# Performance work log

Measured on AMD Instinct MI355X. Metric: run time of the kernel, lower is better.

## Reference

```python
import jax, jax.numpy as jnp
import numpy as np

B, D, H, E, TOPK, NTASK = 16384, 128, 4, 8, 2, 1
ODIM = D // H  # MoE expert output dim (input_feat // num_heads)


def setup_inputs() -> dict:
    key = jax.random.key(0)
    ks = jax.random.split(key, 12)
    s = lambda k, shp, fan: jax.random.normal(k, shp, jnp.float32) / np.sqrt(fan)
    return {
        "x": jax.random.normal(ks[0], (B, D), jnp.float32),
        "Wq": s(ks[1], (D, D * H), D), "bq": jnp.zeros((D * H,), jnp.float32),
        "Wk": s(ks[2], (D, D * H), D), "bk": jnp.zeros((D * H,), jnp.float32),
        "Wg": s(ks[3], (D, E), D),
        "W1": s(ks[4], (E, D, D), D), "b1": jnp.zeros((E, D), jnp.float32),
        "W2": s(ks[5], (E, D, ODIM), D), "b2": jnp.zeros((E, ODIM), jnp.float32),
        "Wout": s(ks[6], (H * ODIM, NTASK), H * ODIM),
        "bout": jnp.zeros((NTASK,), jnp.float32),
    }


def reference(x, Wq, bq, Wk, bk, Wg, W1, b1, W2, b2, Wout, bout):
    # query/key projections -> [B, H, D] token views, flattened to [N, D]
    tok = (x @ Wq + bq).reshape(B * H, D)
    gate_tok = (x @ Wk + bk).reshape(B * H, D)

    # gating: softmax over experts, top-2 routing with renormalized weights
    probs = jax.nn.softmax(gate_tok @ Wg, axis=-1)          # [N, E]
    top_p, top_i = jax.lax.top_k(probs, TOPK)               # [N, k]
    weights = top_p / jnp.sum(top_p, axis=-1, keepdims=True)

    # expert MLPs (dense all-expert compute, then gather selected)
    h = jax.nn.relu(jnp.einsum('nd,edh->neh', tok, W1) + b1)  # [N, E, D]
    eo = jnp.einsum('neh,eho->neo', h, W2) + b2               # [N, E, ODIM]
    sel = jnp.take_along_axis(eo, top_i[:, :, None], axis=1)  # [N, k, ODIM]
    y = jnp.sum(weights[:, :, None] * sel, axis=1)            # [N, ODIM]

    # load-balancing auxiliary loss (switch-style): E * sum(frac_i * mean_prob_i)
    one_hot = jax.nn.one_hot(top_i[:, 0], E, dtype=probs.dtype)
    frac = jnp.mean(one_hot, axis=0)
    mean_p = jnp.mean(probs, axis=0)
    aux_loss = E * jnp.sum(frac * mean_p)

    out = y.reshape(B, H * ODIM) @ Wout + bout                # [B, NTASK]
    return out, aux_loss
```

## Files before the change

kernel.cpp:

```cpp
#include <hip/hip_runtime.h>
#include <hip/hip_bf16.h>

#define BB   16384
#define DD   128
#define HH   4
#define EE   8
#define NN   (BB*HH)
#define OD   32
#define PT   136
#define NL   32
#define CAP2 6144

typedef __attribute__((ext_vector_type(8))) short short8;
typedef __attribute__((ext_vector_type(4))) short short4v;
typedef __attribute__((ext_vector_type(4))) float f32x4;

static __device__ __forceinline__ short f2bf(float v) {
    unsigned int u = __builtin_bit_cast(unsigned int, v);
    u = (u + 0x7FFFu + ((u >> 16) & 1u)) >> 16;
    return (short)u;
}
static __device__ __forceinline__ float bf2f(short b) {
    unsigned int u = ((unsigned int)(unsigned short)b) << 16;
    return __builtin_bit_cast(float, u);
}

__global__ __launch_bounds__(256) void prep_tiny(
    const float* __restrict__ Wk, const float* __restrict__ Wg,
    const float* __restrict__ bk, const float* __restrict__ bout,
    float* __restrict__ Wkg, float* __restrict__ bkg,
    float* __restrict__ out, int* __restrict__ cursors)
{
    int idx = blockIdx.x * 256 + threadIdx.x;
    if (idx < 4096) {
        int k = idx >> 5, col = idx & 31, hh = col >> 3, e = col & 7;
        float s = 0.f;
        #pragma unroll 8
        for (int d = 0; d < 128; ++d) s += Wk[k * 512 + hh * 128 + d] * Wg[d * 8 + e];
        Wkg[k * 32 + col] = s;
    } else if (idx < 4128) {
        int r = idx - 4096;
        int hh = r >> 3, e = r & 7;
        float s = 0.f;
        #pragma unroll 8
        for (int d = 0; d < 128; ++d) s += bk[hh * 128 + d] * Wg[d * 8 + e];
        bkg[r] = s;
    } else if (idx < 20512) {
        out[idx - 4128] = bout[0];
    } else if (idx < 20544) {
        int r = idx - 20512;
        cursors[r] = r * CAP2;
    }
}

__global__ __launch_bounds__(256) void mid(
    const float* __restrict__ x, const float* __restrict__ Wq, const float* __restrict__ bq,
    const float* __restrict__ W1, const float* __restrict__ b1, const float* __restrict__ W2,
    const float* __restrict__ Wkg, const float* __restrict__ bkg,
    short* __restrict__ xb, short* __restrict__ A1F, float* __restrict__ bias1,
    short* __restrict__ W2F, float* __restrict__ wts, float* __restrict__ blkPart,
    int* __restrict__ cursors, int* __restrict__ listIdx)
{
    __shared__ __align__(16) char smemU[34816];
    __shared__ float lps[EE];
    __shared__ float lcn[EE];
    __shared__ int   lcnt[NL];
    __shared__ int   lbase[NL];

    const int blk = blockIdx.x;
    const int t   = threadIdx.x;

    if (blk < 256) {
        float* xL = (float*)smemU;
        const int b0 = blk * 64;

        if (t < EE) { lps[t] = 0.f; lcn[t] = 0.f; }
        if (t < NL) lcnt[t] = 0;

        for (int i = t; i < 2048; i += 256) {
            int r = i >> 5, c = i & 31;
            float4 v = ((const float4*)(x + (size_t)(b0 + r) * 128))[c];
            float* dst = xL + r * 129 + c * 4;
            dst[0] = v.x; dst[1] = v.y; dst[2] = v.z; dst[3] = v.w;
        }
        __syncthreads();

        const int h  = __builtin_amdgcn_readfirstlane(t >> 6);
        const int lb = t & 63;

        const f32x4* wkg4 = (const f32x4*)Wkg;
        f32x4 a0 = ((const f32x4*)bkg)[h * 2];
        f32x4 a1 = ((const f32x4*)bkg)[h * 2 + 1];

        const float* xrow = xL + lb * 129;
        #pragma unroll 4
        for (int k = 0; k < 128; ++k) {
            float xv = xrow[k];
            f32x4 w0 = wkg4[k * 8 + h * 2];
            f32x4 w1 = wkg4[k * 8 + h * 2 + 1];
            a0 += w0 * xv;
            a1 += w1 * xv;
        }

        float l[8] = {a0[0], a0[1], a0[2], a0[3], a1[0], a1[1], a1[2], a1[3]};
        float mx = l[0];
        #pragma unroll
        for (int e = 1; e < 8; ++e) mx = fmaxf(mx, l[e]);
        float p[8]; float sm = 0.f;
        #pragma unroll
        for (int e = 0; e < 8; ++e) { p[e] = __expf(l[e] - mx); sm += p[e]; }
        float isin = 1.f / sm;
        #pragma unroll
        for (int e = 0; e < 8; ++e) p[e] *= isin;

        int i1 = 0; float p1 = p[0];
        #pragma unroll
        for (int e = 1; e < 8; ++e) if (p[e] > p1) { p1 = p[e]; i1 = e; }
        int i2 = (i1 == 0) ? 1 : 0; float p2 = p[i2];
        #pragma unroll
        for (int e = 0; e < 8; ++e) if (e != i1 && p[e] > p2) { p2 = p[e]; i2 = e; }

        int n = (b0 + lb) * 4 + h;
        float rinv = 1.f / (p1 + p2);
        wts[2*n]    = p1 * rinv; wts[2*n+1]  = p2 * rinv;

        int li0 = i1 * 4 + h, li1 = i2 * 4 + h;
        int s0 = atomicAdd(&lcnt[li0], 1);
        int s1 = atomicAdd(&lcnt[li1], 1);

        #pragma unroll
        for (int e = 0; e < 8; ++e) {
            float v = p[e];
            #pragma unroll
            for (int m2 = 1; m2 < 64; m2 <<= 1) v += __shfl_xor(v, m2);
            unsigned long long m1b = __ballot(i1 == e);
            if (lb == 0) {
                atomicAdd(&lps[e], v);
                atomicAdd(&lcn[e], (float)__popcll(m1b));
            }
        }
        __syncthreads();
        if (t < NL) lbase[t] = atomicAdd(&cursors[t], lcnt[t]);
        __syncthreads();

        int q0 = lbase[li0] + s0;
        if (q0 < (li0 + 1) * CAP2) listIdx[q0] = 2*n;
        int q1 = lbase[li1] + s1;
        if (q1 < (li1 + 1) * CAP2) listIdx[q1] = 2*n + 1;

        if (t < EE) {
            float* bp = blkPart + blk * 16;
            bp[t]     = lps[t];
            bp[8 + t] = lcn[t];
        }
    } else if (blk < 288) {
        short* L = (short*)smemU;
        const int li = blk - 256;
        const int e = li >> 2, h = li & 3;
        const int wv = t >> 6, lane = t & 63, l16 = lane & 15, quad = lane >> 4;

        #pragma unroll
        for (int rep = 0; rep < 16; ++rep) {
            int idx = t + rep * 256;
            int c = idx >> 5, h4 = (idx & 31) * 4;
            float4 v = *(const float4*)(W1 + e * 16384 + c * 128 + h4);
            L[(h4 + 0) * PT + c] = f2bf(v.x);
            L[(h4 + 1) * PT + c] = f2bf(v.y);
            L[(h4 + 2) * PT + c] = f2bf(v.z);
            L[(h4 + 3) * PT + c] = f2bf(v.w);
        }
        __syncthreads();

        short8 af[2][4];
        #pragma unroll
        for (int ml = 0; ml < 2; ++ml)
            #pragma unroll
            for (int ks = 0; ks < 4; ++ks)
                af[ml][ks] = *(const short8*)(L + ((wv*2 + ml)*16 + l16) * PT + ks*32 + quad*8);
        if (t < 128) {
            float s = 0.f;
            #pragma unroll 8
            for (int c = 0; c < 128; ++c)
                s += bq[h*128 + c] * bf2f(L[t * PT + c]);
            bias1[li*128 + t] = s + b1[e*128 + t];
        }
        __syncthreads();

        #pragma unroll
        for (int rep = 0; rep < 4; ++rep) {
            int idx = t + rep * 256;
            int d = idx >> 3, c0 = (idx & 7) * 16;
            const float4* src = (const float4*)(Wq + d * 512 + h * 128 + c0);
            float4 v0 = src[0], v1 = src[1], v2 = src[2], v3 = src[3];
            short8 a, b;
            a[0]=f2bf(v0.x); a[1]=f2bf(v0.y); a[2]=f2bf(v0.z); a[3]=f2bf(v0.w);
            a[4]=f2bf(v1.x); a[5]=f2bf(v1.y); a[6]=f2bf(v1.z); a[7]=f2bf(v1.w);
            b[0]=f2bf(v2.x); b[1]=f2bf(v2.y); b[2]=f2bf(v2.z); b[3]=f2bf(v2.w);
            b[4]=f2bf(v3.x); b[5]=f2bf(v3.y); b[6]=f2bf(v3.z); b[7]=f2bf(v3.w);
            *(short8*)(L + d * PT + c0)     = a;
            *(short8*)(L + d * PT + c0 + 8) = b;
        }
        __syncthreads();

        f32x4 acc[2][8];
        #pragma unroll
        for (int ml = 0; ml < 2; ++ml)
            #pragma unroll
            for (int nt2 = 0; nt2 < 8; ++nt2)
                acc[ml][nt2] = (f32x4){0.f, 0.f, 0.f, 0.f};
        #pragma unroll
        for (int ks = 0; ks < 4; ++ks) {
            short8 bfr[8];
            #pragma unroll
            for (int nt2 = 0; nt2 < 8; ++nt2)
                bfr[nt2] = *(const short8*)(L + (nt2*16 + l16) * PT + ks*32 + quad*8);
            #pragma unroll
            for (int ml = 0; ml < 2; ++ml)
                #pragma unroll
                for (int nt2 = 0; nt2 < 8; ++nt2)
                    acc[ml][nt2] = __builtin_amdgcn_mfma_f32_16x16x32_bf16(af[ml][ks], bfr[nt2], acc[ml][nt2], 0, 0, 0);
        }
        __syncthreads();

        #pragma unroll
        for (int ml = 0; ml < 2; ++ml)
            #pragma unroll
            for (int nt2 = 0; nt2 < 8; ++nt2)
                #pragma unroll
                for (int r = 0; r < 4; ++r)
                    L[((wv*2 + ml)*16 + quad*4 + r) * PT + nt2*16 + l16] = f2bf(acc[ml][nt2][r]);
        __syncthreads();

        #pragma unroll
        for (int mt = 0; mt < 8; ++mt)
            #pragma unroll
            for (int ks = 0; ks < 4; ++ks) {
                short8 v = *(const short8*)(L + (mt*16 + l16) * PT + ks*32 + quad*8);
                *(short8*)(A1F + ((size_t)(((li*8 + mt)*4 + ks)*64 + lane)) * 8) = v;
            }
    } else {
        for (int s = blk - 288; s < 1152; s += 896) {
            if (s < 1024) {
                int idx = s * 256 + t;
                const float4* x4 = (const float4*)x;
                float4 v0 = x4[idx * 2], v1 = x4[idx * 2 + 1];
                short8 sv;
                sv[0]=f2bf(v0.x); sv[1]=f2bf(v0.y); sv[2]=f2bf(v0.z); sv[3]=f2bf(v0.w);
                sv[4]=f2bf(v1.x); sv[5]=f2bf(v1.y); sv[6]=f2bf(v1.z); sv[7]=f2bf(v1.w);
                *(short8*)(xb + (size_t)idx * 8) = sv;
            } else {
                int r = (s - 1024) * 256 + t;
                int j = r & 7, lane = (r >> 3) & 63, ks = (r >> 9) & 3, mt = (r >> 11) & 1, e = r >> 12;
                int l16 = lane & 15, quad = lane >> 4;
                int m = mt * 16 + l16, k = ks * 32 + quad * 8 + j;
                W2F[r] = f2bf(W2[e * 4096 + k * 32 + m]);
            }
        }
    }
}

__global__ __launch_bounds__(256) void k2b_expert(
    const short* __restrict__ xb, const short* __restrict__ A1F,
    const float* __restrict__ bias1, const short* __restrict__ W2F, const float* __restrict__ b2,
    const int* __restrict__ cursors, const int* __restrict__ listIdx,
    const float* __restrict__ wts, const float* __restrict__ Wout,
    const float* __restrict__ blkPart, float* __restrict__ out)
{
    __shared__ short tokL[64 * PT];
    __shared__ short hL[64 * PT];
    __shared__ int   ids[64];
    __shared__ float wsl[64];
    __shared__ float red[16][16];
    __shared__ float fin[16];

    const int li = blockIdx.y;
    const int e  = li >> 2;
    const int h  = li & 3;
    const int t  = threadIdx.x;

    if (blockIdx.x == gridDim.x - 1 && li == NL - 1) {
        int chunk = t >> 4, col = t & 15;
        float v = 0.f;
        for (int i = 0; i < 16; ++i) v += blkPart[(chunk * 16 + i) * 16 + col];
        red[chunk][col] = v;
        __syncthreads();
        if (t < 16) {
            float s = 0.f;
            #pragma unroll
            for (int c = 0; c < 16; ++c) s += red[c][t];
            fin[t] = s;
        }
        __syncthreads();
        if (t == 0) {
            float aux = 0.f;
            const float invN = 1.f / (float)NN;
            for (int e2 = 0; e2 < EE; ++e2) aux += (fin[8 + e2] * invN) * (fin[e2] * invN);
            out[BB] = (float)EE * aux;
        }
    }

    int cnt = cursors[li] - li * CAP2;
    if (cnt > CAP2) cnt = CAP2;
    const int off = blockIdx.x * 64;
    if (off >= cnt) return;
    const int sb  = li * CAP2 + off;
    const int nt  = min(64, cnt - off);

    if (t < 64) {
        int a = listIdx[sb + min(t, nt - 1)];
        ids[t] = a >> 3;
        wsl[t] = (t < nt) ? wts[a] : 0.f;
    }
    __syncthreads();

    #pragma unroll
    for (int r = 0; r < 4; ++r) {
        int i = t + r * 256;
        int slot = i >> 4, seg = i & 15;
        short8 v = *(const short8*)(xb + (size_t)ids[slot] * 128 + seg * 8);
        *(short8*)(tokL + slot * PT + seg * 8) = v;
    }
    __syncthreads();

    const int wv   = t >> 6;
    const int lane = t & 63;
    const int l16  = lane & 15;
    const int quad = lane >> 4;

    f32x4 acc[2][4];
    #pragma unroll
    for (int ml = 0; ml < 2; ++ml)
        #pragma unroll
        for (int nl = 0; nl < 4; ++nl)
            acc[ml][nl] = (f32x4){0.f, 0.f, 0.f, 0.f};

    short8 af[2][4];
    #pragma unroll
    for (int ml = 0; ml < 2; ++ml)
        #pragma unroll
        for (int ks = 0; ks < 4; ++ks)
            af[ml][ks] = *(const short8*)(A1F + ((size_t)(((li*8 + wv*2 + ml)*4 + ks)*64 + lane)) * 8);

    short8 bfr[4][4];
    #pragma unroll
    for (int nl = 0; nl < 4; ++nl)
        #pragma unroll
        for (int ks = 0; ks < 4; ++ks)
            bfr[nl][ks] = *(const short8*)(tokL + (nl*16 + l16) * PT + ks*32 + quad*8);

    #pragma unroll
    for (int ks = 0; ks < 4; ++ks)
        #pragma unroll
        for (int ml = 0; ml < 2; ++ml)
            #pragma unroll
            for (int nl = 0; nl < 4; ++nl)
                acc[ml][nl] = __builtin_amdgcn_mfma_f32_16x16x32_bf16(af[ml][ks], bfr[nl][ks], acc[ml][nl], 0, 0, 0);

    #pragma unroll
    for (int ml = 0; ml < 2; ++ml) {
        int hid0 = wv*32 + ml*16 + quad*4;
        f32x4 b1v = *(const f32x4*)(bias1 + li*128 + hid0);
        #pragma unroll
        for (int nl = 0; nl < 4; ++nl) {
            short4v hv;
            #pragma unroll
            for (int r = 0; r < 4; ++r) {
                float v = acc[ml][nl][r] + b1v[r];
                hv[r] = f2bf(fmaxf(v, 0.f));
            }
            *(short4v*)(hL + (nl*16 + l16) * PT + hid0) = hv;
        }
    }
    __syncthreads();

    f32x4 acc2[2];
    acc2[0] = (f32x4){0.f, 0.f, 0.f, 0.f};
    acc2[1] = (f32x4){0.f, 0.f, 0.f, 0.f};

    short8 af2[2][4];
    #pragma unroll
    for (int ml = 0; ml < 2; ++ml)
        #pragma unroll
        for (int ks = 0; ks < 4; ++ks)
            af2[ml][ks] = *(const short8*)(W2F + ((size_t)(((e*2 + ml)*4 + ks)*64 + lane)) * 8);

    short8 bf2[4];
    #pragma unroll
    for (int ks = 0; ks < 4; ++ks)
        bf2[ks] = *(const short8*)(hL + (wv*16 + l16) * PT + ks*32 + quad*8);

    #pragma unroll
    for (int ks = 0; ks < 4; ++ks)
        #pragma unroll
        for (int ml = 0; ml < 2; ++ml)
            acc2[ml] = __builtin_amdgcn_mfma_f32_16x16x32_bf16(af2[ml][ks], bf2[ks], acc2[ml], 0, 0, 0);

    const int slot = wv*16 + l16;
    const int b    = ids[slot];
    float partial = 0.f;
    #pragma unroll
    for (int ml = 0; ml < 2; ++ml) {
        int od0 = ml*16 + quad*4;
        f32x4 b2v = *(const f32x4*)(b2 + e*32 + od0);
        f32x4 wv4 = *(const f32x4*)(Wout + h*32 + od0);
        #pragma unroll
        for (int r = 0; r < 4; ++r)
            partial += (acc2[ml][r] + b2v[r]) * wv4[r];
    }
    partial += __shfl_xor(partial, 16);
    partial += __shfl_xor(partial, 32);
    if (quad == 0) {
        float v = partial * wsl[slot];
        atomicAdd(&out[b], v);
    }
}

extern "C" void kernel_launch(void* const* d_in, const int* in_sizes, int n_in,
                              void* d_out, int out_size, void* d_ws, size_t ws_size,
                              hipStream_t stream) {
    (void)in_sizes; (void)n_in; (void)out_size; (void)ws_size;
    const float* x    = (const float*)d_in[0];
    const float* Wq   = (const float*)d_in[1];
    const float* bq   = (const float*)d_in[2];
    const float* Wk   = (const float*)d_in[3];
    const float* bk   = (const float*)d_in[4];
    const float* Wg   = (const float*)d_in[5];
    const float* W1   = (const float*)d_in[6];
    const float* b1   = (const float*)d_in[7];
    const float* W2   = (const float*)d_in[8];
    const float* b2   = (const float*)d_in[9];
    const float* Wout = (const float*)d_in[10];
    const float* bout = (const float*)d_in[11];
    float* out = (float*)d_out;

    char* ws = (char*)d_ws;
    short* xb       = (short*)(ws + 0);
    float* wts      = (float*)(ws + 4194304);
    int*   listIdx  = (int*)  (ws + 4718592);
    short* A1F      = (short*)(ws + 5505024);
    short* W2F      = (short*)(ws + 6553600);
    float* Wkg      = (float*)(ws + 6619136);
    float* bkg      = (float*)(ws + 6635520);
    float* bias1    = (float*)(ws + 6635648);
    float* blkPart  = (float*)(ws + 6652032);
    int*   cursors  = (int*)  (ws + 6668416);

    prep_tiny<<<81, 256, 0, stream>>>(Wk, Wg, bk, bout, Wkg, bkg, out, cursors);
    mid<<<1184, 256, 0, stream>>>(x, Wq, bq, W1, b1, W2, Wkg, bkg,
                                  xb, A1F, bias1, W2F, wts, blkPart, cursors, listIdx);
    k2b_expert<<<dim3(96, NL), 256, 0, stream>>>(xb, A1F, bias1, W2F, b2,
                                  cursors, listIdx, wts, Wout, blkPart, out);
}
```

Measured before the change: 126.5 us.

## Fold prep kernel into mid: recompute Wk·Wg per block, memset cursors

```diff
diff --git a/kernel.cpp b/kernel.cpp
--- a/kernel.cpp
+++ b/kernel.cpp
@@ -25,43 +25,16 @@
     return __builtin_bit_cast(float, u);
 }
 
-__global__ __launch_bounds__(256) void prep_tiny(
-    const float* __restrict__ Wk, const float* __restrict__ Wg,
-    const float* __restrict__ bk, const float* __restrict__ bout,
-    float* __restrict__ Wkg, float* __restrict__ bkg,
-    float* __restrict__ out, int* __restrict__ cursors)
-{
-    int idx = blockIdx.x * 256 + threadIdx.x;
-    if (idx < 4096) {
-        int k = idx >> 5, col = idx & 31, hh = col >> 3, e = col & 7;
-        float s = 0.f;
-        #pragma unroll 8
-        for (int d = 0; d < 128; ++d) s += Wk[k * 512 + hh * 128 + d] * Wg[d * 8 + e];
-        Wkg[k * 32 + col] = s;
-    } else if (idx < 4128) {
-        int r = idx - 4096;
-        int hh = r >> 3, e = r & 7;
-        float s = 0.f;
-        #pragma unroll 8
-        for (int d = 0; d < 128; ++d) s += bk[hh * 128 + d] * Wg[d * 8 + e];
-        bkg[r] = s;
-    } else if (idx < 20512) {
-        out[idx - 4128] = bout[0];
-    } else if (idx < 20544) {
-        int r = idx - 20512;
-        cursors[r] = r * CAP2;
-    }
-}
-
 __global__ __launch_bounds__(256) void mid(
     const float* __restrict__ x, const float* __restrict__ Wq, const float* __restrict__ bq,
+    const float* __restrict__ Wk, const float* __restrict__ Wg, const float* __restrict__ bk,
     const float* __restrict__ W1, const float* __restrict__ b1, const float* __restrict__ W2,
-    const float* __restrict__ Wkg, const float* __restrict__ bkg,
+    const float* __restrict__ bout,
     short* __restrict__ xb, short* __restrict__ A1F, float* __restrict__ bias1,
     short* __restrict__ W2F, float* __restrict__ wts, float* __restrict__ blkPart,
-    int* __restrict__ cursors, int* __restrict__ listIdx)
+    int* __restrict__ cursors, int* __restrict__ listIdx, float* __restrict__ out)
 {
-    __shared__ __align__(16) char smemU[34816];
+    __shared__ __align__(16) char smemU[53760];
     __shared__ float lps[EE];
     __shared__ float lcn[EE];
     __shared__ int   lcnt[NL];
@@ -71,11 +44,16 @@
     const int t   = threadIdx.x;
 
     if (blk < 256) {
-        float* xL = (float*)smemU;
+        float* xL   = (float*)smemU;
+        f32x4* wg4  = (f32x4*)(smemU + 33024);
+        f32x4* wkgL = (f32x4*)(smemU + 37120);
+        float* bkgL = (float*)(smemU + 53504);
         const int b0 = blk * 64;
 
         if (t < EE) { lps[t] = 0.f; lcn[t] = 0.f; }
         if (t < NL) lcnt[t] = 0;
+
+        ((float4*)wg4)[t] = ((const float4*)Wg)[t];
 
         for (int i = t; i < 2048; i += 256) {
             int r = i >> 5, c = i & 31;
@@ -85,19 +63,45 @@
         }
         __syncthreads();
 
+        #pragma unroll
+        for (int rep = 0; rep < 2; ++rep) {
+            int pi = t + rep * 256;
+            int k = pi >> 2, hh = pi & 3;
+            f32x4 a0 = (f32x4){0.f,0.f,0.f,0.f}, a1v = (f32x4){0.f,0.f,0.f,0.f};
+            const float* wkrow = Wk + k * 512 + hh * 128;
+            #pragma unroll 4
+            for (int d0 = 0; d0 < 128; d0 += 4) {
+                float4 w = *(const float4*)(wkrow + d0);
+                a0 += wg4[(d0+0)*2]   * w.x;  a1v += wg4[(d0+0)*2+1] * w.x;
+                a0 += wg4[(d0+1)*2]   * w.y;  a1v += wg4[(d0+1)*2+1] * w.y;
+                a0 += wg4[(d0+2)*2]   * w.z;  a1v += wg4[(d0+2)*2+1] * w.z;
+                a0 += wg4[(d0+3)*2]   * w.w;  a1v += wg4[(d0+3)*2+1] * w.w;
+            }
+            wkgL[k*8 + hh*2]     = a0;
+            wkgL[k*8 + hh*2 + 1] = a1v;
+        }
+        if (t < 32) {
+            int hh = t >> 3, e = t & 7;
+            const float* wgf = (const float*)wg4;
+            float s = 0.f;
+            #pragma unroll 8
+            for (int d = 0; d < 128; ++d) s += bk[hh*128 + d] * wgf[d*8 + e];
+            bkgL[t] = s;
+        }
+        __syncthreads();
+
         const int h  = __builtin_amdgcn_readfirstlane(t >> 6);
         const int lb = t & 63;
 
-        const f32x4* wkg4 = (const f32x4*)Wkg;
-        f32x4 a0 = ((const f32x4*)bkg)[h * 2];
-        f32x4 a1 = ((const f32x4*)bkg)[h * 2 + 1];
+        f32x4 a0 = ((const f32x4*)bkgL)[h * 2];
+        f32x4 a1 = ((const f32x4*)bkgL)[h * 2 + 1];
 
         const float* xrow = xL + lb * 129;
         #pragma unroll 4
         for (int k = 0; k < 128; ++k) {
             float xv = xrow[k];
-            f32x4 w0 = wkg4[k * 8 + h * 2];
-            f32x4 w1 = wkg4[k * 8 + h * 2 + 1];
+            f32x4 w0 = wkgL[k * 8 + h * 2];
+            f32x4 w1 = wkgL[k * 8 + h * 2 + 1];
             a0 += w0 * xv;
             a1 += w1 * xv;
         }
@@ -143,9 +147,9 @@
         if (t < NL) lbase[t] = atomicAdd(&cursors[t], lcnt[t]);
         __syncthreads();
 
-        int q0 = lbase[li0] + s0;
+        int q0 = li0 * CAP2 + lbase[li0] + s0;
         if (q0 < (li0 + 1) * CAP2) listIdx[q0] = 2*n;
-        int q1 = lbase[li1] + s1;
+        int q1 = li1 * CAP2 + lbase[li1] + s1;
         if (q1 < (li1 + 1) * CAP2) listIdx[q1] = 2*n + 1;
 
         if (t < EE) {
@@ -239,7 +243,7 @@
                 *(short8*)(A1F + ((size_t)(((li*8 + mt)*4 + ks)*64 + lane)) * 8) = v;
             }
     } else {
-        for (int s = blk - 288; s < 1152; s += 896) {
+        for (int s = blk - 288; s < 1216; s += 896) {
             if (s < 1024) {
                 int idx = s * 256 + t;
                 const float4* x4 = (const float4*)x;
@@ -248,12 +252,14 @@
                 sv[0]=f2bf(v0.x); sv[1]=f2bf(v0.y); sv[2]=f2bf(v0.z); sv[3]=f2bf(v0.w);
                 sv[4]=f2bf(v1.x); sv[5]=f2bf(v1.y); sv[6]=f2bf(v1.z); sv[7]=f2bf(v1.w);
                 *(short8*)(xb + (size_t)idx * 8) = sv;
-            } else {
+            } else if (s < 1152) {
                 int r = (s - 1024) * 256 + t;
                 int j = r & 7, lane = (r >> 3) & 63, ks = (r >> 9) & 3, mt = (r >> 11) & 1, e = r >> 12;
                 int l16 = lane & 15, quad = lane >> 4;
                 int m = mt * 16 + l16, k = ks * 32 + quad * 8 + j;
                 W2F[r] = f2bf(W2[e * 4096 + k * 32 + m]);
+            } else {
+                out[(s - 1152) * 256 + t] = bout[0];
             }
         }
     }
@@ -299,7 +305,7 @@
         }
     }
 
-    int cnt = cursors[li] - li * CAP2;
+    int cnt = cursors[li];
     if (cnt > CAP2) cnt = CAP2;
     const int off = blockIdx.x * 64;
     if (off >= cnt) return;
@@ -439,15 +445,13 @@
     int*   listIdx  = (int*)  (ws + 4718592);
     short* A1F      = (short*)(ws + 5505024);
     short* W2F      = (short*)(ws + 6553600);
-    float* Wkg      = (float*)(ws + 6619136);
-    float* bkg      = (float*)(ws + 6635520);
     float* bias1    = (float*)(ws + 6635648);
     float* blkPart  = (float*)(ws + 6652032);
     int*   cursors  = (int*)  (ws + 6668416);
 
-    prep_tiny<<<81, 256, 0, stream>>>(Wk, Wg, bk, bout, Wkg, bkg, out, cursors);
-    mid<<<1184, 256, 0, stream>>>(x, Wq, bq, W1, b1, W2, Wkg, bkg,
-                                  xb, A1F, bias1, W2F, wts, blkPart, cursors, listIdx);
+    hipMemsetAsync(cursors, 0, NL * sizeof(int), stream);
+    mid<<<1184, 256, 0, stream>>>(x, Wq, bq, Wk, Wg, bk, W1, b1, W2, bout,
+                                  xb, A1F, bias1, W2F, wts, blkPart, cursors, listIdx, out);
     k2b_expert<<<dim3(96, NL), 256, 0, stream>>>(xb, A1F, bias1, W2F, b2,
                                   cursors, listIdx, wts, Wout, blkPart, out);
 }
```

After: 124.9 us. Within noise of the previous version (-1.3%).
